# Optimization experiments

Hardware: AMD Instinct MI355X
Metric: run time of the kernel (lower is better)

## Reference

```python
import jax, jax.numpy as jnp
import numpy as np

N, D = 16384, 32
RHO = 0.01  # default Scalar(0.01) in make()


def setup_inputs() -> dict:
    key = jax.random.key(0)
    k1, k2, k3, k4, k5 = jax.random.split(key, 5)
    return {
        "mus": jax.random.normal(k1, (N, D), dtype=jnp.float32),
        "W1": jax.random.normal(k2, (D, D), dtype=jnp.float32),  # Linear(dim, dim), stored [in, out]
        "b1": jax.random.normal(k3, (D,), dtype=jnp.float32),
        "W2": jax.random.normal(k4, (D, 1), dtype=jnp.float32),  # Linear(dim, 1), stored [in, out]
        "b2": jax.random.normal(k5, (1,), dtype=jnp.float32),
    }


def reference(mus, W1, b1, W2, b2):
    n, d = mus.shape
    rho = jnp.float32(RHO)
    sigma2 = jnp.float32(1.0)  # sigma = 1 hardcoded in kernel()
    # scalar prefactor, computed in fp32 like the torch module
    term1 = (2.0 * rho) ** (d / 2.0)
    term2 = (2.0 * jnp.float32(np.pi) * sigma2) ** ((1.0 - 2.0 * rho) * d / 2.0)
    # pairwise squared euclidean distances: ||mu_i - mu_j||^2, [N, N]
    sq = jnp.sum(mus * mus, axis=1)
    sqd = jnp.maximum(sq[:, None] + sq[None, :] - 2.0 * (mus @ mus.T), 0.0)
    L = term1 * term2 * jnp.exp(-rho * sqd / (4.0 * sigma2))
    # focalization: exp(MLP(mu)) added to the diagonal
    foc = jnp.exp(jnp.tanh(mus @ W1 + b1) @ W2 + b2)[:, 0]  # [N]
    idx = jnp.arange(n)
    return L.at[idx, idx].add(foc)
```

## Files before the change

### kernel.cpp

```cpp
#include <hip/hip_runtime.h>
#include <math.h>


#define NROW 16384
#define DIM 32

typedef _Float16 f16x8 __attribute__((ext_vector_type(8)));
typedef float f32x16 __attribute__((ext_vector_type(16)));

__global__ __launch_bounds__(64) void lens_prep(
    const float* __restrict__ mus, const float* __restrict__ W1,
    const float* __restrict__ b1, const float* __restrict__ W2,
    const float* __restrict__ b2, _Float16* __restrict__ mf,
    float* __restrict__ sq, float* __restrict__ foc) {
  const int i = blockIdx.x * blockDim.x + threadIdx.x;
  if (i >= NROW) return;

  float row[DIM];
  const float4* rp = reinterpret_cast<const float4*>(mus + (size_t)i * DIM);
#pragma unroll
  for (int q = 0; q < DIM / 4; ++q) {
    float4 v = rp[q];
    row[q * 4 + 0] = v.x;
    row[q * 4 + 1] = v.y;
    row[q * 4 + 2] = v.z;
    row[q * 4 + 3] = v.w;
  }

  float s = 0.0f;
  f16x8 h[4];
#pragma unroll
  for (int q = 0; q < 4; ++q) {
#pragma unroll
    for (int e = 0; e < 8; ++e) {
      _Float16 hv = (_Float16)row[q * 8 + e];
      h[q][e] = hv;
      float f = (float)hv;
      s = fmaf(f, f, s);
    }
  }
  f16x8* mp = reinterpret_cast<f16x8*>(mf + (size_t)i * DIM);
  mp[0] = h[0];
  mp[1] = h[1];
  mp[2] = h[2];
  mp[3] = h[3];
  sq[i] = s;

  float acc2 = 0.0f;
#pragma unroll 4
  for (int j = 0; j < DIM; ++j) {
    float hj = b1[j];
#pragma unroll
    for (int k = 0; k < DIM; ++k) hj = fmaf(row[k], W1[k * DIM + j], hj);
    acc2 = fmaf(tanhf(hj), W2[j], acc2);
  }
  foc[i] = __expf(acc2 + b2[0]);
}

__global__ __launch_bounds__(256) void lens_main(
    const _Float16* __restrict__ mf, const float* __restrict__ sq,
    const float* __restrict__ foc, float* __restrict__ out,
    float scale, float k1) {
  const int tid = threadIdx.x;
  const int lane = tid & 63;
  const int w = tid >> 6;
  const int wr = w >> 1, wc = w & 1;
  const int lo = lane & 31, hi = lane >> 5;
  const int rbase = blockIdx.y * 128 + wr * 64;
  const int cbase = blockIdx.x * 128 + wc * 64;
  const bool diagblock = (blockIdx.x == blockIdx.y);

  f16x8 af[2][2], bf[2][2];
#pragma unroll
  for (int s = 0; s < 2; ++s) {
#pragma unroll
    for (int kh = 0; kh < 2; ++kh) {
      af[s][kh] = *reinterpret_cast<const f16x8*>(
          mf + (size_t)(rbase + s * 32 + lo) * DIM + kh * 16 + hi * 8);
      bf[s][kh] = *reinterpret_cast<const f16x8*>(
          mf + (size_t)(cbase + s * 32 + lo) * DIM + kh * 16 + hi * 8);
    }
  }

  float sqc[2];
#pragma unroll
  for (int sc = 0; sc < 2; ++sc) sqc[sc] = sq[cbase + sc * 32 + lo];

#pragma unroll
  for (int sr = 0; sr < 2; ++sr) {
    const int r0 = rbase + sr * 32 + hi * 4;
    float sqr[16];
#pragma unroll
    for (int r = 0; r < 16; ++r) sqr[r] = sq[r0 + (r & 3) + 8 * (r >> 2)];
#pragma unroll
    for (int sc = 0; sc < 2; ++sc) {
      f32x16 c;
#pragma unroll
      for (int e = 0; e < 16; ++e) c[e] = 0.0f;
      c = __builtin_amdgcn_mfma_f32_32x32x16_f16(af[sr][0], bf[sc][0], c, 0, 0, 0);
      c = __builtin_amdgcn_mfma_f32_32x32x16_f16(af[sr][1], bf[sc][1], c, 0, 0, 0);

      const int col = cbase + sc * 32 + lo;
      const float sc2 = sqc[sc];
#pragma unroll
      for (int r = 0; r < 16; ++r) {
        const int row = r0 + (r & 3) + 8 * (r >> 2);
        float t = sqr[r] + sc2 - 2.0f * c[r];
        t = fmaxf(t, 0.0f);
        float v = scale * __expf(k1 * t);
        if (diagblock && row == col) v += foc[row];
        __builtin_nontemporal_store(v, &out[(size_t)row * NROW + col]);
      }
    }
  }
}

extern "C" void kernel_launch(void* const* d_in, const int* in_sizes, int n_in,
                              void* d_out, int out_size, void* d_ws, size_t ws_size,
                              hipStream_t stream) {
  const float* mus = (const float*)d_in[0];
  const float* W1 = (const float*)d_in[1];
  const float* b1 = (const float*)d_in[2];
  const float* W2 = (const float*)d_in[3];
  const float* b2 = (const float*)d_in[4];
  float* out = (float*)d_out;

  char* ws = (char*)d_ws;
  _Float16* mf = (_Float16*)ws;
  float* sq = (float*)(ws + (size_t)NROW * DIM * 2);
  float* foc = (float*)(ws + (size_t)NROW * DIM * 2 + NROW * 4);

  const double rho = 0.01, dd = (double)DIM;
  const double pi = 3.14159265358979323846;
  const double term1 = pow(2.0 * rho, dd / 2.0);
  const double term2 = pow(2.0 * pi, (1.0 - 2.0 * rho) * dd / 2.0);
  const float scale = (float)(term1 * term2);
  const float k1 = (float)(-rho / 4.0);

  lens_prep<<<NROW / 64, 64, 0, stream>>>(mus, W1, b1, W2, b2, mf, sq, foc);

  dim3 grid(NROW / 128, NROW / 128);
  lens_main<<<grid, 256, 0, stream>>>(mf, sq, foc, out, scale, k1);
}
```

Baseline: 219.3 us.

## Swap MFMA operands for row-contiguous float4 stores and fold scale into exp2

The MFMA operands are swapped so that each lane owns one output row and holds four consecutive columns. This allows float4 stores instead of scalar nontemporal stores. The scale prefactor and the log2e factor are folded into a single exp2 argument computed with an FMA, with precomputed per-row and per-column terms, and fmin replaces the clamp at zero. This removes per-element multiplies and many per-row loads, and should improve write coalescing for the memory-bound 1 GiB output. The plain stores drop the nontemporal hint.

```diff
diff --git a/kernel.cpp b/kernel.cpp
--- a/kernel.cpp
+++ b/kernel.cpp
@@ -60,7 +60,7 @@
 __global__ __launch_bounds__(256) void lens_main(
     const _Float16* __restrict__ mf, const float* __restrict__ sq,
     const float* __restrict__ foc, float* __restrict__ out,
-    float scale, float k1) {
+    float k2, float lgscale) {
   const int tid = threadIdx.x;
   const int lane = tid & 63;
   const int w = tid >> 6;
@@ -69,6 +69,7 @@
   const int rbase = blockIdx.y * 128 + wr * 64;
   const int cbase = blockIdx.x * 128 + wc * 64;
   const bool diagblock = (blockIdx.x == blockIdx.y);
+  const float m2k2 = -2.0f * k2;
 
   f16x8 af[2][2], bf[2][2];
 #pragma unroll
@@ -82,34 +83,55 @@
     }
   }
 
-  float sqc[2];
+  float4 bb[2][4];
 #pragma unroll
-  for (int sc = 0; sc < 2; ++sc) sqc[sc] = sq[cbase + sc * 32 + lo];
+  for (int sc = 0; sc < 2; ++sc) {
+#pragma unroll
+    for (int g = 0; g < 4; ++g) {
+      float4 sv = *reinterpret_cast<const float4*>(
+          &sq[cbase + sc * 32 + 4 * hi + 8 * g]);
+      bb[sc][g].x = sv.x * k2;
+      bb[sc][g].y = sv.y * k2;
+      bb[sc][g].z = sv.z * k2;
+      bb[sc][g].w = sv.w * k2;
+    }
+  }
 
 #pragma unroll
   for (int sr = 0; sr < 2; ++sr) {
-    const int r0 = rbase + sr * 32 + hi * 4;
-    float sqr[16];
-#pragma unroll
-    for (int r = 0; r < 16; ++r) sqr[r] = sq[r0 + (r & 3) + 8 * (r >> 2)];
+    const int R = rbase + sr * 32 + lo;
+    const float a = fmaf(sq[R], k2, lgscale);
+    float focv = 0.0f;
+    if (diagblock) focv = foc[R];
+    float* orow = out + (size_t)R * NROW + cbase + 4 * hi;
+
 #pragma unroll
     for (int sc = 0; sc < 2; ++sc) {
       f32x16 c;
 #pragma unroll
       for (int e = 0; e < 16; ++e) c[e] = 0.0f;
-      c = __builtin_amdgcn_mfma_f32_32x32x16_f16(af[sr][0], bf[sc][0], c, 0, 0, 0);
-      c = __builtin_amdgcn_mfma_f32_32x32x16_f16(af[sr][1], bf[sc][1], c, 0, 0, 0);
+      c = __builtin_amdgcn_mfma_f32_32x32x16_f16(bf[sc][0], af[sr][0], c, 0, 0, 0);
+      c = __builtin_amdgcn_mfma_f32_32x32x16_f16(bf[sc][1], af[sr][1], c, 0, 0, 0);
 
-      const int col = cbase + sc * 32 + lo;
-      const float sc2 = sqc[sc];
 #pragma unroll
-      for (int r = 0; r < 16; ++r) {
-        const int row = r0 + (r & 3) + 8 * (r >> 2);
-        float t = sqr[r] + sc2 - 2.0f * c[r];
-        t = fmaxf(t, 0.0f);
-        float v = scale * __expf(k1 * t);
-        if (diagblock && row == col) v += foc[row];
-        __builtin_nontemporal_store(v, &out[(size_t)row * NROW + col]);
+      for (int g = 0; g < 4; ++g) {
+        float4 o;
+        o.x = __builtin_amdgcn_exp2f(
+            fminf(fmaf(c[4 * g + 0], m2k2, a + bb[sc][g].x), lgscale));
+        o.y = __builtin_amdgcn_exp2f(
+            fminf(fmaf(c[4 * g + 1], m2k2, a + bb[sc][g].y), lgscale));
+        o.z = __builtin_amdgcn_exp2f(
+            fminf(fmaf(c[4 * g + 2], m2k2, a + bb[sc][g].z), lgscale));
+        o.w = __builtin_amdgcn_exp2f(
+            fminf(fmaf(c[4 * g + 3], m2k2, a + bb[sc][g].w), lgscale));
+        if (diagblock) {
+          const int C = cbase + sc * 32 + 4 * hi + 8 * g;
+          if (R == C + 0) o.x += focv;
+          if (R == C + 1) o.y += focv;
+          if (R == C + 2) o.z += focv;
+          if (R == C + 3) o.w += focv;
+        }
+        *reinterpret_cast<float4*>(orow + sc * 32 + 8 * g) = o;
       }
     }
   }
@@ -132,13 +154,14 @@
 
   const double rho = 0.01, dd = (double)DIM;
   const double pi = 3.14159265358979323846;
-  const double term1 = pow(2.0 * rho, dd / 2.0);
-  const double term2 = pow(2.0 * pi, (1.0 - 2.0 * rho) * dd / 2.0);
-  const float scale = (float)(term1 * term2);
-  const float k1 = (float)(-rho / 4.0);
+  const double log2e = 1.4426950408889634;
+  const double lg_d = (dd / 2.0) * (log(2.0 * rho) * log2e) +
+                      ((1.0 - 2.0 * rho) * dd / 2.0) * (log(2.0 * pi) * log2e);
+  const float k2 = (float)(-(rho / 4.0) * log2e);
+  const float lgscale = (float)lg_d;
 
   lens_prep<<<NROW / 64, 64, 0, stream>>>(mus, W1, b1, W2, b2, mf, sq, foc);
 
   dim3 grid(NROW / 128, NROW / 128);
-  lens_main<<<grid, 256, 0, stream>>>(mf, sq, foc, out, scale, k1);
+  lens_main<<<grid, 256, 0, stream>>>(mf, sq, foc, out, k2, lgscale);
 }
```

Result: slower. 228.9 us (+4.4%).

## Stream full row strips per block and fold scale into exp2 exponent

Applied to the files above, without the earlier changes.

Replaces the 2D 128x128 tiling with one block per 32-row strip, where each of 8 waves walks 2048 columns and reloads B fragments per 32-column step. It precomputes per-row terms and folds the scalar prefactor into the exponent as a log2 offset, using a single exp2 with a clamp in place of the max and multiply. The prep kernel block size also changes. The output is a write-bound 1 GB store, so this mainly cuts launch and instruction overhead; the risk is fewer blocks and changed store access patterns.

```diff
diff --git a/kernel.cpp b/kernel.cpp
--- a/kernel.cpp
+++ b/kernel.cpp
@@ -4,11 +4,13 @@
 
 #define NROW 16384
 #define DIM 32
+#define ROWS 32
+#define WCOLS 2048
 
 typedef _Float16 f16x8 __attribute__((ext_vector_type(8)));
 typedef float f32x16 __attribute__((ext_vector_type(16)));
 
-__global__ __launch_bounds__(64) void lens_prep(
+__global__ __launch_bounds__(256) void lens_prep(
     const float* __restrict__ mus, const float* __restrict__ W1,
     const float* __restrict__ b1, const float* __restrict__ W2,
     const float* __restrict__ b2, _Float16* __restrict__ mf,
@@ -57,60 +59,57 @@
   foc[i] = __expf(acc2 + b2[0]);
 }
 
-__global__ __launch_bounds__(256) void lens_main(
+__global__ __launch_bounds__(512) void lens_main(
     const _Float16* __restrict__ mf, const float* __restrict__ sq,
     const float* __restrict__ foc, float* __restrict__ out,
-    float scale, float k1) {
+    float k2, float lgscale) {
   const int tid = threadIdx.x;
   const int lane = tid & 63;
   const int w = tid >> 6;
-  const int wr = w >> 1, wc = w & 1;
   const int lo = lane & 31, hi = lane >> 5;
-  const int rbase = blockIdx.y * 128 + wr * 64;
-  const int cbase = blockIdx.x * 128 + wc * 64;
-  const bool diagblock = (blockIdx.x == blockIdx.y);
+  const int rbase = blockIdx.x * ROWS;
+  const int c0base = w * WCOLS;
+  const float m2k2 = -2.0f * k2;
 
-  f16x8 af[2][2], bf[2][2];
+  f16x8 af[2];
 #pragma unroll
-  for (int s = 0; s < 2; ++s) {
+  for (int kh = 0; kh < 2; ++kh)
+    af[kh] = *reinterpret_cast<const f16x8*>(
+        mf + (size_t)(rbase + lo) * DIM + kh * 16 + hi * 8);
+
+  float ar[16];
+  float* rowp[16];
 #pragma unroll
-    for (int kh = 0; kh < 2; ++kh) {
-      af[s][kh] = *reinterpret_cast<const f16x8*>(
-          mf + (size_t)(rbase + s * 32 + lo) * DIM + kh * 16 + hi * 8);
-      bf[s][kh] = *reinterpret_cast<const f16x8*>(
-          mf + (size_t)(cbase + s * 32 + lo) * DIM + kh * 16 + hi * 8);
-    }
+  for (int r = 0; r < 16; ++r) {
+    const int row = rbase + (r & 3) + 8 * (r >> 2) + 4 * hi;
+    ar[r] = fmaf(sq[row], k2, lgscale);
+    rowp[r] = out + (size_t)row * NROW;
   }
 
-  float sqc[2];
+#pragma unroll 4
+  for (int sc = 0; sc < WCOLS / 32; ++sc) {
+    const int c0 = c0base + sc * 32;
+
+    f16x8 bf0 = *reinterpret_cast<const f16x8*>(
+        mf + (size_t)(c0 + lo) * DIM + hi * 8);
+    f16x8 bf1 = *reinterpret_cast<const f16x8*>(
+        mf + (size_t)(c0 + lo) * DIM + 16 + hi * 8);
+    const float bcol = sq[c0 + lo] * k2;
+
+    f32x16 c;
 #pragma unroll
-  for (int sc = 0; sc < 2; ++sc) sqc[sc] = sq[cbase + sc * 32 + lo];
+    for (int e = 0; e < 16; ++e) c[e] = 0.0f;
+    c = __builtin_amdgcn_mfma_f32_32x32x16_f16(af[0], bf0, c, 0, 0, 0);
+    c = __builtin_amdgcn_mfma_f32_32x32x16_f16(af[1], bf1, c, 0, 0, 0);
 
+    const bool diag = (c0 == rbase);
 #pragma unroll
-  for (int sr = 0; sr < 2; ++sr) {
-    const int r0 = rbase + sr * 32 + hi * 4;
-    float sqr[16];
-#pragma unroll
-    for (int r = 0; r < 16; ++r) sqr[r] = sq[r0 + (r & 3) + 8 * (r >> 2)];
-#pragma unroll
-    for (int sc = 0; sc < 2; ++sc) {
-      f32x16 c;
-#pragma unroll
-      for (int e = 0; e < 16; ++e) c[e] = 0.0f;
-      c = __builtin_amdgcn_mfma_f32_32x32x16_f16(af[sr][0], bf[sc][0], c, 0, 0, 0);
-      c = __builtin_amdgcn_mfma_f32_32x32x16_f16(af[sr][1], bf[sc][1], c, 0, 0, 0);
-
-      const int col = cbase + sc * 32 + lo;
-      const float sc2 = sqc[sc];
-#pragma unroll
-      for (int r = 0; r < 16; ++r) {
-        const int row = r0 + (r & 3) + 8 * (r >> 2);
-        float t = sqr[r] + sc2 - 2.0f * c[r];
-        t = fmaxf(t, 0.0f);
-        float v = scale * __expf(k1 * t);
-        if (diagblock && row == col) v += foc[row];
-        __builtin_nontemporal_store(v, &out[(size_t)row * NROW + col]);
-      }
+    for (int r = 0; r < 16; ++r) {
+      float v = __builtin_amdgcn_exp2f(
+          fminf(fmaf(c[r], m2k2, ar[r] + bcol), lgscale));
+      if (diag && lo == ((r & 3) + 8 * (r >> 2) + 4 * hi))
+        v += foc[rbase + lo];
+      __builtin_nontemporal_store(v, rowp[r] + c0 + lo);
     }
   }
 }
@@ -132,13 +131,13 @@
 
   const double rho = 0.01, dd = (double)DIM;
   const double pi = 3.14159265358979323846;
-  const double term1 = pow(2.0 * rho, dd / 2.0);
-  const double term2 = pow(2.0 * pi, (1.0 - 2.0 * rho) * dd / 2.0);
-  const float scale = (float)(term1 * term2);
-  const float k1 = (float)(-rho / 4.0);
+  const double log2e = 1.4426950408889634;
+  const double lg_d = (dd / 2.0) * (log(2.0 * rho) * log2e) +
+                      ((1.0 - 2.0 * rho) * dd / 2.0) * (log(2.0 * pi) * log2e);
+  const float k2 = (float)(-(rho / 4.0) * log2e);
+  const float lgscale = (float)lg_d;
 
-  lens_prep<<<NROW / 64, 64, 0, stream>>>(mus, W1, b1, W2, b2, mf, sq, foc);
+  lens_prep<<<NROW / 256, 256, 0, stream>>>(mus, W1, b1, W2, b2, mf, sq, foc);
 
-  dim3 grid(NROW / 128, NROW / 128);
-  lens_main<<<grid, 256, 0, stream>>>(mf, sq, foc, out, scale, k1);
+  lens_main<<<NROW / ROWS, 512, 0, stream>>>(mf, sq, foc, out, k2, lgscale);
 }
```

After: 275.7 us. 1.26x slower.
